# Kernel optimization log

Hardware: AMD Instinct MI355X
Metric: run time of the kernel (lower is better)

## Reference

```python
import jax, jax.numpy as jnp
import numpy as np

N = 100000
E = 3200000
IN_C = 128
HID = 128


def setup_inputs() -> dict:
    key = jax.random.key(0)
    k1, k2, k3, k4, k5 = jax.random.split(key, 5)
    x = jax.random.normal(k1, (N, IN_C), dtype=jnp.float32)
    edge_index = jax.random.randint(k2, (2, E), 0, N, dtype=jnp.int64)
    edge_weight = jax.random.uniform(k3, (E,), dtype=jnp.float32)
    # GCNConv linear weight [out, in] (applied as x @ W.T), glorot-ish scale
    W = jax.random.normal(k4, (HID, IN_C), dtype=jnp.float32) / np.sqrt(IN_C)
    bias = jnp.zeros((HID,), dtype=jnp.float32)
    # PReLU per-channel alpha, torch default init 0.25
    alpha = jnp.full((HID,), 0.25, dtype=jnp.float32)
    return {"x": x, "edge_index": edge_index, "edge_weight": edge_weight,
            "W": W, "bias": bias, "alpha": alpha}


def reference(x, edge_index, edge_weight, W, bias, alpha):
    n = x.shape[0]
    # gcn_norm with self-loops (fill value 1.0)
    loop_idx = jnp.arange(n, dtype=edge_index.dtype)
    row = jnp.concatenate([edge_index[0], loop_idx])  # source
    col = jnp.concatenate([edge_index[1], loop_idx])  # target
    ew = jnp.concatenate([edge_weight, jnp.ones((n,), dtype=edge_weight.dtype)])
    deg = jax.ops.segment_sum(ew, col, num_segments=n)  # in-degree by weight
    dinv = jnp.where(deg > 0, jax.lax.rsqrt(deg), 0.0)
    norm = dinv[row] * ew * dinv[col]  # [E+N]
    # linear transform first (GCNConv order), then gather-scatter aggregation
    h = x @ W.T  # [N, HID]
    msgs = norm[:, None] * h[row]  # [E+N, HID]
    out = jax.ops.segment_sum(msgs, col, num_segments=n) + bias  # [N, HID]
    # PReLU with per-channel alpha
    return jnp.where(out > 0, out, alpha * out)
```

## Files before the change

kernel.cpp:

```cpp
#include <hip/hip_runtime.h>


#define NBLK    512
#define MAXBKT  2048
#define EPB     6250
#define QSCALE  32767.0f
#define Q9      511.0f
#define SBS     16

typedef float vfloat2 __attribute__((ext_vector_type(2)));

__device__ __forceinline__ unsigned bf16pack2(float a, float b) {
    unsigned ua = __float_as_uint(a);
    ua = (ua + 0x7fffu + ((ua >> 16) & 1u)) >> 16;
    unsigned ub = __float_as_uint(b);
    ub = (ub + 0x7fffu + ((ub >> 16) & 1u)) >> 16;
    return ua | (ub << 16);
}

__device__ __forceinline__ float2 bf16unpack2(unsigned u) {
    return make_float2(__uint_as_float(u << 16),
                       __uint_as_float(u & 0xffff0000u));
}

__device__ __forceinline__ int chunk_swz(int bid) {
    return (bid & 7) * (NBLK / 8) + (bid >> 3);
}

__global__ __launch_bounds__(256) void p1_hist(const int* __restrict__ col,
                                               unsigned* __restrict__ hist,
                                               int e, int nbkt, int epb) {
    __shared__ unsigned lh[MAXBKT];
    int c = chunk_swz(blockIdx.x);
    int t = threadIdx.x;
    for (int k = t; k < nbkt; k += 256) lh[k] = 0;
    __syncthreads();
    int s = c * epb, en = s + epb; if (en > e) en = e;
    for (int i = s + t; i < en; i += 256)
        atomicAdd(&lh[__builtin_nontemporal_load(&col[i]) >> 6], 1u);
    __syncthreads();
    for (int k = t; k < nbkt; k += 256)
        hist[(size_t)k * NBLK + c] = lh[k];
}

__global__ __launch_bounds__(1024) void scan_partial2(
    const unsigned* __restrict__ a, unsigned* __restrict__ part, int m) {
    __shared__ unsigned red[1024];
    int t = threadIdx.x, i = blockIdx.x * 1024 + t;
    red[t] = (i < m) ? a[i] : 0;
    __syncthreads();
    #pragma unroll
    for (int d = 512; d > 0; d >>= 1) {
        if (t < d) red[t] += red[t + d];
        __syncthreads();
    }
    if (t == 0) part[blockIdx.x] = red[0];
}

__global__ __launch_bounds__(1024) void scan_base2(
    unsigned* __restrict__ part, int nb, int* __restrict__ offs, int n, int e) {
    __shared__ unsigned s[1024];
    int t = threadIdx.x;
    unsigned v = (t < nb) ? part[t] : 0;
    s[t] = v;
    __syncthreads();
    for (int d = 1; d < 1024; d <<= 1) {
        unsigned add = (t >= d) ? s[t - d] : 0;
        __syncthreads();
        s[t] += add;
        __syncthreads();
    }
    if (t < nb) part[t] = s[t] - v;
    if (t == 0) offs[n] = e;
}

__global__ __launch_bounds__(1024) void scan_write2(
    unsigned* __restrict__ a, const unsigned* __restrict__ part, int m) {
    __shared__ unsigned s[1024];
    int t = threadIdx.x, i = blockIdx.x * 1024 + t;
    unsigned v = (i < m) ? a[i] : 0;
    s[t] = v;
    __syncthreads();
    for (int d = 1; d < 1024; d <<= 1) {
        unsigned add = (t >= d) ? s[t - d] : 0;
        __syncthreads();
        s[t] += add;
        __syncthreads();
    }
    if (i < m) a[i] = part[blockIdx.x] + s[t] - v;
}

__global__ __launch_bounds__(512) void fused_p2_gemm(
    const int* __restrict__ col, const int* __restrict__ row,
    const float* __restrict__ ew, const unsigned* __restrict__ base,
    unsigned* __restrict__ pay, int e, int nbkt, int epb, int m,
    const float* __restrict__ x, const float* __restrict__ W,
    unsigned* __restrict__ h, int n, int nblocks) {
    __shared__ unsigned smem[16384];
    int bid = blockIdx.x;
    int t = threadIdx.x;
    unsigned p2b = (unsigned)(((unsigned long long)bid * NBLK) / nblocks);
    bool isP2 = ((((unsigned long long)(bid + 1) * NBLK) / nblocks) > p2b);

    if (isP2) {
        unsigned* lcnt  = smem;
        unsigned* lcur  = smem + 2048;
        unsigned* lbase = smem + 4096;
        unsigned* sums  = smem + 6144;
        unsigned* pay_l = smem + 6656;
        unsigned short* bk_l = (unsigned short*)(smem + 12906);

        int c0 = (int)p2b;
        for (int k = t; k < MAXBKT; k += 512) { lcnt[k] = 0; lcur[k] = 0; }
        __syncthreads();
        for (int k = t; k < nbkt; k += 512) {
            size_t f = (size_t)k * NBLK + c0;
            unsigned b  = base[f];
            unsigned nx = (f + 1 < (size_t)m) ? base[f + 1] : (unsigned)e;
            lbase[k] = b;
            lcnt[k]  = nx - b;
        }
        __syncthreads();

        int s0 = c0 * epb, en = s0 + epb; if (en > e) en = e;
        int cnt_tot = en - s0;

        unsigned loc0, loc1, loc2, loc3, ls;
        {
            int b0 = t * 4;
            loc0 = lcnt[b0]; loc1 = lcnt[b0 + 1];
            loc2 = lcnt[b0 + 2]; loc3 = lcnt[b0 + 3];
            ls = loc0 + loc1 + loc2 + loc3;
            sums[t] = ls;
        }
        __syncthreads();
        for (int d = 1; d < 512; d <<= 1) {
            unsigned add = (t >= d) ? sums[t - d] : 0;
            __syncthreads();
            sums[t] += add;
            __syncthreads();
        }
        {
            unsigned run = sums[t] - ls;
            int b0 = t * 4;
            lcnt[b0] = run;           run += loc0;
            lcnt[b0 + 1] = run;       run += loc1;
            lcnt[b0 + 2] = run;       run += loc2;
            lcnt[b0 + 3] = run;
        }
        __syncthreads();

        for (int i = s0 + t; i < en; i += 512) {
            int c = __builtin_nontemporal_load(&col[i]);
            int r = __builtin_nontemporal_load(&row[i]);
            float w = __builtin_nontemporal_load(&ew[i]);
            int bk = c >> 6;
            unsigned q = (unsigned)(w * Q9 + 0.5f);
            unsigned rk = atomicAdd(&lcur[bk], 1u);
            unsigned sl = lcnt[bk] + rk;
            pay_l[sl] = ((unsigned)(c & 63) << 26) | ((unsigned)r << 9) | q;
            bk_l[sl] = (unsigned short)bk;
        }
        __syncthreads();

        for (int sl = t; sl < cnt_tot; sl += 512) {
            int bk = (int)bk_l[sl];
            unsigned g = lbase[bk] + (sl - lcnt[bk]);
            pay[g] = pay_l[sl];
        }
        return;
    }

    int gidx = bid - (int)p2b;
    float (*Wt)[128] = (float (*)[128])smem;
    const float4* W4 = (const float4*)W;
    #pragma unroll
    for (int it = 0; it < 8; ++it) {
        int i = t + it * 512;
        float4 v = W4[i];
        int o  = i >> 5;
        int kb = (i & 31) << 2;
        Wt[kb + 0][o ^ (((kb + 0) & 7) << 2)] = v.x;
        Wt[kb + 1][o ^ (((kb + 1) & 7) << 2)] = v.y;
        Wt[kb + 2][o ^ (((kb + 2) & 7) << 2)] = v.z;
        Wt[kb + 3][o ^ (((kb + 3) & 7) << 2)] = v.w;
    }
    __syncthreads();

    int tc = t & 31;
    int rs = t >> 5;
    int r0 = gidx * 128 + rs * 8;
    if (r0 >= n) return;
    const float4* x4 = (const float4*)x;

    float acc[8][4];
    #pragma unroll
    for (int ri = 0; ri < 8; ++ri)
        #pragma unroll
        for (int j = 0; j < 4; ++j) acc[ri][j] = 0.0f;

    int rcnt = n - r0; if (rcnt > 8) rcnt = 8;

    if (rcnt == 8) {
        for (int kq = 0; kq < 32; ++kq) {
            int kb = kq << 2;
            float4 wv0 = *(const float4*)&Wt[kb + 0][(4 * tc) ^ (((kb + 0) & 7) << 2)];
            float4 wv1 = *(const float4*)&Wt[kb + 1][(4 * tc) ^ (((kb + 1) & 7) << 2)];
            float4 wv2 = *(const float4*)&Wt[kb + 2][(4 * tc) ^ (((kb + 2) & 7) << 2)];
            float4 wv3 = *(const float4*)&Wt[kb + 3][(4 * tc) ^ (((kb + 3) & 7) << 2)];
            #pragma unroll
            for (int ri = 0; ri < 8; ++ri) {
                float4 xv = x4[(size_t)(r0 + ri) * 32 + kq];
                acc[ri][0] += xv.x * wv0.x + xv.y * wv1.x + xv.z * wv2.x + xv.w * wv3.x;
                acc[ri][1] += xv.x * wv0.y + xv.y * wv1.y + xv.z * wv2.y + xv.w * wv3.y;
                acc[ri][2] += xv.x * wv0.z + xv.y * wv1.z + xv.z * wv2.z + xv.w * wv3.z;
                acc[ri][3] += xv.x * wv0.w + xv.y * wv1.w + xv.z * wv2.w + xv.w * wv3.w;
            }
        }
        uint2* h2 = (uint2*)h;
        #pragma unroll
        for (int ri = 0; ri < 8; ++ri)
            h2[(size_t)(r0 + ri) * 32 + tc] =
                make_uint2(bf16pack2(acc[ri][0], acc[ri][1]),
                           bf16pack2(acc[ri][2], acc[ri][3]));
    } else {
        for (int kq = 0; kq < 32; ++kq) {
            int kb = kq << 2;
            float4 wv0 = *(const float4*)&Wt[kb + 0][(4 * tc) ^ (((kb + 0) & 7) << 2)];
            float4 wv1 = *(const float4*)&Wt[kb + 1][(4 * tc) ^ (((kb + 1) & 7) << 2)];
            float4 wv2 = *(const float4*)&Wt[kb + 2][(4 * tc) ^ (((kb + 2) & 7) << 2)];
            float4 wv3 = *(const float4*)&Wt[kb + 3][(4 * tc) ^ (((kb + 3) & 7) << 2)];
            for (int ri = 0; ri < rcnt; ++ri) {
                float4 xv = x4[(size_t)(r0 + ri) * 32 + kq];
                acc[ri][0] += xv.x * wv0.x + xv.y * wv1.x + xv.z * wv2.x + xv.w * wv3.x;
                acc[ri][1] += xv.x * wv0.y + xv.y * wv1.y + xv.z * wv2.y + xv.w * wv3.y;
                acc[ri][2] += xv.x * wv0.z + xv.y * wv1.z + xv.z * wv2.z + xv.w * wv3.z;
                acc[ri][3] += xv.x * wv0.w + xv.y * wv1.w + xv.z * wv2.w + xv.w * wv3.w;
            }
        }
        uint2* h2 = (uint2*)h;
        for (int ri = 0; ri < rcnt; ++ri)
            h2[(size_t)(r0 + ri) * 32 + tc] =
                make_uint2(bf16pack2(acc[ri][0], acc[ri][1]),
                           bf16pack2(acc[ri][2], acc[ri][3]));
    }
}

__global__ __launch_bounds__(256) void p3a_stats(
    const unsigned* __restrict__ pay, const unsigned* __restrict__ histBase,
    unsigned short* __restrict__ lofsT, int* __restrict__ offs,
    float* __restrict__ dinv, int n, int nbkt, int e) {
    __shared__ unsigned cnt[64][SBS];
    __shared__ unsigned wsum[64], tbase[64], ttot[64];
    int bk = blockIdx.x;
    int zs = (int)histBase[(size_t)bk * NBLK];
    int ze = (bk + 1 < nbkt) ? (int)histBase[(size_t)(bk + 1) * NBLK] : e;
    int t = threadIdx.x;
    for (int k = t; k < 64 * SBS; k += 256) (&cnt[0][0])[k] = 0;
    if (t < 64) wsum[t] = 0;
    __syncthreads();
    for (int p = zs + t; p < ze; p += 256) {
        unsigned v = pay[p];
        int l = (int)(v >> 26);
        int sb = (int)(((v >> 9) & 0x1ffffu) >> 13);
        atomicAdd(&cnt[l][sb], 1u);
        atomicAdd(&wsum[l], v & 0x1ffu);
    }
    __syncthreads();
    if (t < 64) {
        unsigned s = 0;
        #pragma unroll
        for (int j = 0; j < SBS; ++j) s += cnt[t][j];
        ttot[t] = s;
    }
    __syncthreads();
    if (t == 0) {
        unsigned run = 0;
        for (int l = 0; l < 64; ++l) { tbase[l] = run; run += ttot[l]; }
    }
    __syncthreads();
    if (t < 64) {
        unsigned run = tbase[t];
        unsigned short* dst = lofsT + ((size_t)bk * 64 + t) * SBS;
        #pragma unroll
        for (int j = 0; j < SBS; ++j) { dst[j] = (unsigned short)run; run += cnt[t][j]; }
        int node = bk * 64 + t;
        if (node < n) {
            offs[node] = zs + (int)tbase[t];
            float dg = 1.0f + (float)wsum[t] * (1.0f / Q9);
            dinv[node] = rsqrtf(dg);
        }
    }
}

__global__ __launch_bounds__(256) void p3b_scatter(
    const unsigned* __restrict__ pay, const unsigned* __restrict__ histBase,
    const unsigned short* __restrict__ lofsT, const float* __restrict__ dinv,
    unsigned* __restrict__ csr2, int nbkt, int e) {
    __shared__ unsigned lofs[64][SBS];
    __shared__ unsigned cur[64][SBS];
    int bk = blockIdx.x;
    int zs = (int)histBase[(size_t)bk * NBLK];
    int ze = (bk + 1 < nbkt) ? (int)histBase[(size_t)(bk + 1) * NBLK] : e;
    int t = threadIdx.x;
    for (int k = t; k < 64 * SBS; k += 256) {
        (&lofs[0][0])[k] = lofsT[(size_t)bk * 64 * SBS + k];
        (&cur[0][0])[k] = 0;
    }
    __syncthreads();
    for (int p = zs + t; p < ze; p += 256) {
        unsigned v = pay[p];
        int l = (int)(v >> 26);
        unsigned src = (v >> 9) & 0x1ffffu;
        int sb = (int)(src >> 13);
        unsigned rk = atomicAdd(&cur[l][sb], 1u);
        float a = dinv[src] * ((float)(v & 0x1ffu) * (1.0f / Q9));
        csr2[zs + lofs[l][sb] + rk] =
            (src << 15) | (unsigned)(a * QSCALE + 0.5f);
    }
}

__global__ __launch_bounds__(256) void aggregate_kernel(
    const unsigned* __restrict__ h, const unsigned* __restrict__ csr2,
    const int* __restrict__ offs, const float* __restrict__ dinv,
    const float* __restrict__ bias, const float* __restrict__ alpha,
    float* __restrict__ out, int n, int swzq) {
    int bid = blockIdx.x;
    int sb  = swzq ? ((bid & 7) * swzq + (bid >> 3)) : bid;
    int w = sb * 4 + (threadIdx.x >> 6);
    if (w >= n) return;
    int lane = threadIdx.x & 63;

    int beg = __builtin_amdgcn_readfirstlane(offs[w]);
    int end = __builtin_amdgcn_readfirstlane(offs[w + 1]);
    float ax = 0.0f, ay = 0.0f;

    int i = beg;
    int end4 = beg + ((end - beg) & ~3);
    for (; i < end4; i += 4) {
        unsigned v0 = csr2[i];
        unsigned v1 = csr2[i + 1];
        unsigned v2 = csr2[i + 2];
        unsigned v3 = csr2[i + 3];
        unsigned u0 = h[(size_t)(v0 >> 15) * 64 + lane];
        unsigned u1 = h[(size_t)(v1 >> 15) * 64 + lane];
        unsigned u2 = h[(size_t)(v2 >> 15) * 64 + lane];
        unsigned u3 = h[(size_t)(v3 >> 15) * 64 + lane];
        float a0 = (float)(v0 & 0x7fffu) * (1.0f / QSCALE);
        float a1 = (float)(v1 & 0x7fffu) * (1.0f / QSCALE);
        float a2 = (float)(v2 & 0x7fffu) * (1.0f / QSCALE);
        float a3 = (float)(v3 & 0x7fffu) * (1.0f / QSCALE);
        float2 h0 = bf16unpack2(u0), h1 = bf16unpack2(u1);
        float2 h2 = bf16unpack2(u2), h3 = bf16unpack2(u3);
        ax += a0 * h0.x; ay += a0 * h0.y;
        ax += a1 * h1.x; ay += a1 * h1.y;
        ax += a2 * h2.x; ay += a2 * h2.y;
        ax += a3 * h3.x; ay += a3 * h3.y;
    }
    for (; i < end; ++i) {
        unsigned v = csr2[i];
        unsigned u = h[(size_t)(v >> 15) * 64 + lane];
        float a = (float)(v & 0x7fffu) * (1.0f / QSCALE);
        float2 hv = bf16unpack2(u);
        ax += a * hv.x; ay += a * hv.y;
    }

    float dc = dinv[w];
    float2 hc = bf16unpack2(h[(size_t)w * 64 + lane]);
    ax += dc * hc.x; ay += dc * hc.y;

    float2 bv = ((const float2*)bias)[lane];
    float2 av = ((const float2*)alpha)[lane];
    float ox = ax * dc + bv.x;
    float oy = ay * dc + bv.y;
    ox = ox > 0.0f ? ox : av.x * ox;
    oy = oy > 0.0f ? oy : av.y * oy;
    vfloat2 ov; ov.x = ox; ov.y = oy;
    __builtin_nontemporal_store(ov,
        (vfloat2*)&((float2*)out)[(size_t)w * 64 + lane]);
}

extern "C" void kernel_launch(void* const* d_in, const int* in_sizes, int n_in,
                              void* d_out, int out_size, void* d_ws, size_t ws_size,
                              hipStream_t stream) {
    const float* x     = (const float*)d_in[0];
    const int*   ei    = (const int*)d_in[1];
    const float* ew    = (const float*)d_in[2];
    const float* W     = (const float*)d_in[3];
    const float* bias  = (const float*)d_in[4];
    const float* alpha = (const float*)d_in[5];
    float* out = (float*)d_out;

    const int n = in_sizes[0] / 128;
    const int e = in_sizes[1] / 2;
    const int* row = ei;
    const int* col = ei + e;

    const int nbkt = (n + 63) >> 6;
    const int m    = nbkt * NBLK;
    const int epb  = (e + NBLK - 1) / NBLK;
    const int nb2  = (m + 1023) / 1024;

    char* ws = (char*)d_ws;
    size_t off = 0;
    auto alloc = [&](size_t bytes) -> char* {
        char* p = ws + off;
        off = (off + bytes + 255) & ~(size_t)255;
        return p;
    };
    unsigned*       hist  = (unsigned*)      alloc((size_t)m * 4);
    unsigned*       part  = (unsigned*)      alloc((size_t)1024 * 4);
    int*            offs  = (int*)           alloc((size_t)(n + 1) * 4);
    float*          dinv  = (float*)         alloc((size_t)n * 4);
    unsigned*       pay   = (unsigned*)      alloc((size_t)e * 4);
    unsigned short* lofsT = (unsigned short*)alloc((size_t)nbkt * 64 * SBS * 2);
    unsigned*       csr2  = (unsigned*)      alloc((size_t)e * 4);
    unsigned*       h     = (unsigned*)      alloc((size_t)n * 128 * 2);
    (void)ws_size; (void)n_in; (void)out_size;

    int gg = (n + 127) / 128;
    int nblocks = NBLK + gg;

    p1_hist<<<NBLK, 256, 0, stream>>>(col, hist, e, nbkt, epb);
    scan_partial2<<<nb2, 1024, 0, stream>>>(hist, part, m);
    scan_base2<<<1, 1024, 0, stream>>>(part, nb2, offs, n, e);
    scan_write2<<<nb2, 1024, 0, stream>>>(hist, part, m);
    fused_p2_gemm<<<nblocks, 512, 0, stream>>>(col, row, ew, hist, pay,
                                               e, nbkt, epb, m, x, W, h, n,
                                               nblocks);
    p3a_stats<<<nbkt, 256, 0, stream>>>(pay, hist, lofsT, offs, dinv,
                                        n, nbkt, e);
    p3b_scatter<<<nbkt, 256, 0, stream>>>(pay, hist, lofsT, dinv, csr2,
                                          nbkt, e);

    int ga = (n + 3) / 4;
    int swzq = (ga % 8 == 0) ? ga / 8 : 0;
    aggregate_kernel<<<ga, 256, 0, stream>>>(h, csr2, offs, dinv,
                                             bias, alpha, out, n, swzq);
}
```

Baseline: 325.2 us.

## Split fused sort-scatter/GEMM kernel into separate p2 and GEMM launches

Replaces the fused kernel that interleaved edge sort-scatter blocks with GEMM blocks by two separate kernels: a dedicated p2_sort_scatter launched with NBLK blocks and a standalone gemm_kernel launched after the p3 stages. This removes the per-block role dispatch and lets each kernel size its own shared memory. In exchange it gives up the concurrent overlap of the dense GEMM with the memory-bound sort phase and adds a kernel launch. It also introduces a chunk swizzle for the p2 block-to-chunk mapping.

Measured after the change: 268.6 us. 17.4% less time.

```diff
diff --git a/kernel.cpp b/kernel.cpp
--- a/kernel.cpp
+++ b/kernel.cpp
@@ -4,6 +4,7 @@
 #define NBLK    512
 #define MAXBKT  2048
 #define EPB     6250
+#define P2T     512
 #define QSCALE  32767.0f
 #define Q9      511.0f
 #define SBS     16
@@ -90,89 +91,157 @@
     if (i < m) a[i] = part[blockIdx.x] + s[t] - v;
 }
 
-__global__ __launch_bounds__(512) void fused_p2_gemm(
+__global__ __launch_bounds__(P2T) void p2_sort_scatter(
     const int* __restrict__ col, const int* __restrict__ row,
     const float* __restrict__ ew, const unsigned* __restrict__ base,
-    unsigned* __restrict__ pay, int e, int nbkt, int epb, int m,
-    const float* __restrict__ x, const float* __restrict__ W,
-    unsigned* __restrict__ h, int n, int nblocks) {
-    __shared__ unsigned smem[16384];
-    int bid = blockIdx.x;
-    int t = threadIdx.x;
-    unsigned p2b = (unsigned)(((unsigned long long)bid * NBLK) / nblocks);
-    bool isP2 = ((((unsigned long long)(bid + 1) * NBLK) / nblocks) > p2b);
-
-    if (isP2) {
-        unsigned* lcnt  = smem;
-        unsigned* lcur  = smem + 2048;
-        unsigned* lbase = smem + 4096;
-        unsigned* sums  = smem + 6144;
-        unsigned* pay_l = smem + 6656;
-        unsigned short* bk_l = (unsigned short*)(smem + 12906);
-
-        int c0 = (int)p2b;
-        for (int k = t; k < MAXBKT; k += 512) { lcnt[k] = 0; lcur[k] = 0; }
-        __syncthreads();
-        for (int k = t; k < nbkt; k += 512) {
-            size_t f = (size_t)k * NBLK + c0;
-            unsigned b  = base[f];
-            unsigned nx = (f + 1 < (size_t)m) ? base[f + 1] : (unsigned)e;
-            lbase[k] = b;
-            lcnt[k]  = nx - b;
+    unsigned* __restrict__ pay, int e, int nbkt, int epb, int m) {
+    __shared__ unsigned lcnt[MAXBKT];
+    __shared__ unsigned lcur[MAXBKT];
+    __shared__ unsigned lbase[MAXBKT];
+    __shared__ unsigned sums[P2T];
+    __shared__ unsigned pay_l[EPB];
+    __shared__ unsigned short bk_l[EPB];
+
+    int c0 = chunk_swz(blockIdx.x);
+    int t = threadIdx.x;
+    for (int k = t; k < MAXBKT; k += P2T) { lcnt[k] = 0; lcur[k] = 0; }
+    __syncthreads();
+    for (int k = t; k < nbkt; k += P2T) {
+        size_t f = (size_t)k * NBLK + c0;
+        unsigned b  = base[f];
+        unsigned nx = (f + 1 < (size_t)m) ? base[f + 1] : (unsigned)e;
+        lbase[k] = b;
+        lcnt[k]  = nx - b;
+    }
+    __syncthreads();
+
+    int s0 = c0 * epb, en = s0 + epb; if (en > e) en = e;
+    int cnt_tot = en - s0;
+
+    unsigned loc0, loc1, loc2, loc3, ls;
+    {
+        int b0 = t * 4;
+        loc0 = lcnt[b0]; loc1 = lcnt[b0 + 1];
+        loc2 = lcnt[b0 + 2]; loc3 = lcnt[b0 + 3];
+        ls = loc0 + loc1 + loc2 + loc3;
+        sums[t] = ls;
+    }
+    __syncthreads();
+    for (int d = 1; d < P2T; d <<= 1) {
+        unsigned add = (t >= d) ? sums[t - d] : 0;
+        __syncthreads();
+        sums[t] += add;
+        __syncthreads();
+    }
+    {
+        unsigned run = sums[t] - ls;
+        int b0 = t * 4;
+        lcnt[b0] = run;           run += loc0;
+        lcnt[b0 + 1] = run;       run += loc1;
+        lcnt[b0 + 2] = run;       run += loc2;
+        lcnt[b0 + 3] = run;
+    }
+    __syncthreads();
+
+    for (int i = s0 + t; i < en; i += P2T) {
+        int c = __builtin_nontemporal_load(&col[i]);
+        int r = __builtin_nontemporal_load(&row[i]);
+        float w = __builtin_nontemporal_load(&ew[i]);
+        int bk = c >> 6;
+        unsigned q = (unsigned)(w * Q9 + 0.5f);
+        unsigned rk = atomicAdd(&lcur[bk], 1u);
+        unsigned sl = lcnt[bk] + rk;
+        pay_l[sl] = ((unsigned)(c & 63) << 26) | ((unsigned)r << 9) | q;
+        bk_l[sl] = (unsigned short)bk;
+    }
+    __syncthreads();
+
+    for (int sl = t; sl < cnt_tot; sl += P2T) {
+        int bk = (int)bk_l[sl];
+        unsigned g = lbase[bk] + (sl - lcnt[bk]);
+        pay[g] = pay_l[sl];
+    }
+}
+
+__global__ __launch_bounds__(256) void p3a_stats(
+    const unsigned* __restrict__ pay, const unsigned* __restrict__ histBase,
+    unsigned short* __restrict__ lofsT, int* __restrict__ offs,
+    float* __restrict__ dinv, int n, int nbkt, int e) {
+    __shared__ unsigned cnt[64][SBS];
+    __shared__ unsigned wsum[64], tbase[64], ttot[64];
+    int bk = blockIdx.x;
+    int zs = (int)histBase[(size_t)bk * NBLK];
+    int ze = (bk + 1 < nbkt) ? (int)histBase[(size_t)(bk + 1) * NBLK] : e;
+    int t = threadIdx.x;
+    for (int k = t; k < 64 * SBS; k += 256) (&cnt[0][0])[k] = 0;
+    if (t < 64) wsum[t] = 0;
+    __syncthreads();
+    for (int p = zs + t; p < ze; p += 256) {
+        unsigned v = pay[p];
+        int l = (int)(v >> 26);
+        int sb = (int)(((v >> 9) & 0x1ffffu) >> 13);
+        atomicAdd(&cnt[l][sb], 1u);
+        atomicAdd(&wsum[l], v & 0x1ffu);
+    }
+    __syncthreads();
+    if (t < 64) {
+        unsigned s = 0;
+        #pragma unroll
+        for (int j = 0; j < SBS; ++j) s += cnt[t][j];
+        ttot[t] = s;
+    }
+    __syncthreads();
+    if (t == 0) {
+        unsigned run = 0;
+        for (int l = 0; l < 64; ++l) { tbase[l] = run; run += ttot[l]; }
+    }
+    __syncthreads();
+    if (t < 64) {
+        unsigned run = tbase[t];
+        unsigned short* dst = lofsT + ((size_t)bk * 64 + t) * SBS;
+        #pragma unroll
+        for (int j = 0; j < SBS; ++j) { dst[j] = (unsigned short)run; run += cnt[t][j]; }
+        int node = bk * 64 + t;
+        if (node < n) {
+            offs[node] = zs + (int)tbase[t];
+            float dg = 1.0f + (float)wsum[t] * (1.0f / Q9);
+            dinv[node] = rsqrtf(dg);
         }
-        __syncthreads();
-
-        int s0 = c0 * epb, en = s0 + epb; if (en > e) en = e;
-        int cnt_tot = en - s0;
-
-        unsigned loc0, loc1, loc2, loc3, ls;
-        {
-            int b0 = t * 4;
-            loc0 = lcnt[b0]; loc1 = lcnt[b0 + 1];
-            loc2 = lcnt[b0 + 2]; loc3 = lcnt[b0 + 3];
-            ls = loc0 + loc1 + loc2 + loc3;
-            sums[t] = ls;
-        }
-        __syncthreads();
-        for (int d = 1; d < 512; d <<= 1) {
-            unsigned add = (t >= d) ? sums[t - d] : 0;
-            __syncthreads();
-            sums[t] += add;
-            __syncthreads();
-        }
-        {
-            unsigned run = sums[t] - ls;
-            int b0 = t * 4;
-            lcnt[b0] = run;           run += loc0;
-            lcnt[b0 + 1] = run;       run += loc1;
-            lcnt[b0 + 2] = run;       run += loc2;
-            lcnt[b0 + 3] = run;
-        }
-        __syncthreads();
-
-        for (int i = s0 + t; i < en; i += 512) {
-            int c = __builtin_nontemporal_load(&col[i]);
-            int r = __builtin_nontemporal_load(&row[i]);
-            float w = __builtin_nontemporal_load(&ew[i]);
-            int bk = c >> 6;
-            unsigned q = (unsigned)(w * Q9 + 0.5f);
-            unsigned rk = atomicAdd(&lcur[bk], 1u);
-            unsigned sl = lcnt[bk] + rk;
-            pay_l[sl] = ((unsigned)(c & 63) << 26) | ((unsigned)r << 9) | q;
-            bk_l[sl] = (unsigned short)bk;
-        }
-        __syncthreads();
-
-        for (int sl = t; sl < cnt_tot; sl += 512) {
-            int bk = (int)bk_l[sl];
-            unsigned g = lbase[bk] + (sl - lcnt[bk]);
-            pay[g] = pay_l[sl];
-        }
-        return;
-    }
-
-    int gidx = bid - (int)p2b;
-    float (*Wt)[128] = (float (*)[128])smem;
+    }
+}
+
+__global__ __launch_bounds__(256) void p3b_scatter(
+    const unsigned* __restrict__ pay, const unsigned* __restrict__ histBase,
+    const unsigned short* __restrict__ lofsT, const float* __restrict__ dinv,
+    unsigned* __restrict__ csr2, int nbkt, int e) {
+    __shared__ unsigned lofs[64][SBS];
+    __shared__ unsigned cur[64][SBS];
+    int bk = blockIdx.x;
+    int zs = (int)histBase[(size_t)bk * NBLK];
+    int ze = (bk + 1 < nbkt) ? (int)histBase[(size_t)(bk + 1) * NBLK] : e;
+    int t = threadIdx.x;
+    for (int k = t; k < 64 * SBS; k += 256) {
+        (&lofs[0][0])[k] = lofsT[(size_t)bk * 64 * SBS + k];
+        (&cur[0][0])[k] = 0;
+    }
+    __syncthreads();
+    for (int p = zs + t; p < ze; p += 256) {
+        unsigned v = pay[p];
+        int l = (int)(v >> 26);
+        unsigned src = (v >> 9) & 0x1ffffu;
+        int sb = (int)(src >> 13);
+        unsigned rk = atomicAdd(&cur[l][sb], 1u);
+        float a = dinv[src] * ((float)(v & 0x1ffu) * (1.0f / Q9));
+        csr2[zs + lofs[l][sb] + rk] =
+            (src << 15) | (unsigned)(a * QSCALE + 0.5f);
+    }
+}
+
+__global__ __launch_bounds__(512) void gemm_kernel(const float* __restrict__ x,
+                                                   const float* __restrict__ W,
+                                                   unsigned* __restrict__ h, int n) {
+    __shared__ float Wt[128][128];
+    int t = threadIdx.x;
     const float4* W4 = (const float4*)W;
     #pragma unroll
     for (int it = 0; it < 8; ++it) {
@@ -189,7 +258,7 @@
 
     int tc = t & 31;
     int rs = t >> 5;
-    int r0 = gidx * 128 + rs * 8;
+    int r0 = blockIdx.x * 128 + rs * 8;
     if (r0 >= n) return;
     const float4* x4 = (const float4*)x;
 
@@ -246,80 +315,6 @@
     }
 }
 
-__global__ __launch_bounds__(256) void p3a_stats(
-    const unsigned* __restrict__ pay, const unsigned* __restrict__ histBase,
-    unsigned short* __restrict__ lofsT, int* __restrict__ offs,
-    float* __restrict__ dinv, int n, int nbkt, int e) {
-    __shared__ unsigned cnt[64][SBS];
-    __shared__ unsigned wsum[64], tbase[64], ttot[64];
-    int bk = blockIdx.x;
-    int zs = (int)histBase[(size_t)bk * NBLK];
-    int ze = (bk + 1 < nbkt) ? (int)histBase[(size_t)(bk + 1) * NBLK] : e;
-    int t = threadIdx.x;
-    for (int k = t; k < 64 * SBS; k += 256) (&cnt[0][0])[k] = 0;
-    if (t < 64) wsum[t] = 0;
-    __syncthreads();
-    for (int p = zs + t; p < ze; p += 256) {
-        unsigned v = pay[p];
-        int l = (int)(v >> 26);
-        int sb = (int)(((v >> 9) & 0x1ffffu) >> 13);
-        atomicAdd(&cnt[l][sb], 1u);
-        atomicAdd(&wsum[l], v & 0x1ffu);
-    }
-    __syncthreads();
-    if (t < 64) {
-        unsigned s = 0;
-        #pragma unroll
-        for (int j = 0; j < SBS; ++j) s += cnt[t][j];
-        ttot[t] = s;
-    }
-    __syncthreads();
-    if (t == 0) {
-        unsigned run = 0;
-        for (int l = 0; l < 64; ++l) { tbase[l] = run; run += ttot[l]; }
-    }
-    __syncthreads();
-    if (t < 64) {
-        unsigned run = tbase[t];
-        unsigned short* dst = lofsT + ((size_t)bk * 64 + t) * SBS;
-        #pragma unroll
-        for (int j = 0; j < SBS; ++j) { dst[j] = (unsigned short)run; run += cnt[t][j]; }
-        int node = bk * 64 + t;
-        if (node < n) {
-            offs[node] = zs + (int)tbase[t];
-            float dg = 1.0f + (float)wsum[t] * (1.0f / Q9);
-            dinv[node] = rsqrtf(dg);
-        }
-    }
-}
-
-__global__ __launch_bounds__(256) void p3b_scatter(
-    const unsigned* __restrict__ pay, const unsigned* __restrict__ histBase,
-    const unsigned short* __restrict__ lofsT, const float* __restrict__ dinv,
-    unsigned* __restrict__ csr2, int nbkt, int e) {
-    __shared__ unsigned lofs[64][SBS];
-    __shared__ unsigned cur[64][SBS];
-    int bk = blockIdx.x;
-    int zs = (int)histBase[(size_t)bk * NBLK];
-    int ze = (bk + 1 < nbkt) ? (int)histBase[(size_t)(bk + 1) * NBLK] : e;
-    int t = threadIdx.x;
-    for (int k = t; k < 64 * SBS; k += 256) {
-        (&lofs[0][0])[k] = lofsT[(size_t)bk * 64 * SBS + k];
-        (&cur[0][0])[k] = 0;
-    }
-    __syncthreads();
-    for (int p = zs + t; p < ze; p += 256) {
-        unsigned v = pay[p];
-        int l = (int)(v >> 26);
-        unsigned src = (v >> 9) & 0x1ffffu;
-        int sb = (int)(src >> 13);
-        unsigned rk = atomicAdd(&cur[l][sb], 1u);
-        float a = dinv[src] * ((float)(v & 0x1ffu) * (1.0f / Q9));
-        csr2[zs + lofs[l][sb] + rk] =
-            (src << 15) | (unsigned)(a * QSCALE + 0.5f);
-    }
-}
-
 __global__ __launch_bounds__(256) void aggregate_kernel(
     const unsigned* __restrict__ h, const unsigned* __restrict__ csr2,
     const int* __restrict__ offs, const float* __restrict__ dinv,
@@ -418,21 +413,20 @@
     unsigned*       h     = (unsigned*)      alloc((size_t)n * 128 * 2);
     (void)ws_size; (void)n_in; (void)out_size;
 
-    int gg = (n + 127) / 128;
-    int nblocks = NBLK + gg;
-
     p1_hist<<<NBLK, 256, 0, stream>>>(col, hist, e, nbkt, epb);
     scan_partial2<<<nb2, 1024, 0, stream>>>(hist, part, m);
     scan_base2<<<1, 1024, 0, stream>>>(part, nb2, offs, n, e);
     scan_write2<<<nb2, 1024, 0, stream>>>(hist, part, m);
-    fused_p2_gemm<<<nblocks, 512, 0, stream>>>(col, row, ew, hist, pay,
-                                               e, nbkt, epb, m, x, W, h, n,
-                                               nblocks);
+    p2_sort_scatter<<<NBLK, P2T, 0, stream>>>(col, row, ew, hist, pay,
+                                              e, nbkt, epb, m);
     p3a_stats<<<nbkt, 256, 0, stream>>>(pay, hist, lofsT, offs, dinv,
                                         n, nbkt, e);
     p3b_scatter<<<nbkt, 256, 0, stream>>>(pay, hist, lofsT, dinv, csr2,
                                           nbkt, e);
 
+    int gg = (n + 127) / 128;
+    gemm_kernel<<<gg, 512, 0, stream>>>(x, W, h, n);
+
     int ga = (n + 3) / 4;
     int swzq = (ga % 8 == 0) ? ga / 8 : 0;
     aggregate_kernel<<<ga, 256, 0, stream>>>(h, csr2, offs, dinv,
```
